# Optimization experiments

Hardware: AMD Instinct MI355X
Metric: run time of the kernel (lower is better)

The kernel has to match this reference:

```python
import jax, jax.numpy as jnp
import numpy as np

D_MODEL = 256
D_STATE = 32
D_CONV = 16
EXPAND = 4
N_LAYERS = 4
D_INNER = EXPAND * D_MODEL  # 1024
DT_RANK = 16  # ceil(d_model / 16)
INPUT_DIM = 78
BATCH = 4096
EPS = 1e-5


def setup_inputs() -> dict:
    key = jax.random.key(0)
    ks = jax.random.split(key, 10)
    f = lambda k, shape, s: jax.random.normal(k, shape, jnp.float32) * s
    return {
        "x": f(ks[0], (BATCH, INPUT_DIM), 1.0),
        "W_proj_in": f(ks[1], (INPUT_DIM, D_MODEL), 0.1),
        "b_proj_in": jnp.zeros((D_MODEL,), jnp.float32),
        "norm_w": jnp.ones((N_LAYERS, D_MODEL), jnp.float32),
        "W_in": f(ks[2], (N_LAYERS, D_MODEL, 2 * D_INNER), 0.05),
        "conv_w": f(ks[3], (N_LAYERS, D_INNER, D_CONV), 0.2),
        "conv_b": jnp.zeros((N_LAYERS, D_INNER), jnp.float32),
        "W_x": f(ks[4], (N_LAYERS, D_INNER, DT_RANK + 2 * D_STATE), 0.03),
        "W_dt": f(ks[5], (N_LAYERS, DT_RANK, D_INNER), 0.1),
        "b_dt": f(ks[6], (N_LAYERS, D_INNER), 0.1),
        "A_log": jnp.log(jnp.broadcast_to(jnp.arange(1, D_STATE + 1, dtype=jnp.float32), (N_LAYERS, D_INNER, D_STATE))),
        "D": jnp.ones((N_LAYERS, D_INNER), jnp.float32),
        "W_out": f(ks[7], (N_LAYERS, D_INNER, D_MODEL), 0.03),
        "W_final": f(ks[8], (D_MODEL, 1), 0.06),
        "b_final": jnp.zeros((1,), jnp.float32),
    }


def _rmsnorm(x, w):
    return x * jax.lax.rsqrt(jnp.mean(x * x, axis=-1, keepdims=True) + EPS) * w


def _causal_dwconv(x, w, b):
    # x: [B, L, ED], w: [ED, K] depthwise causal conv (left pad K-1)
    lhs = jnp.transpose(x, (0, 2, 1))                 # [B, ED, L]
    rhs = w[:, None, :]                               # [ED, 1, K]
    out = jax.lax.conv_general_dilated(lhs, rhs, (1,), [(D_CONV - 1, 0)], feature_group_count=D_INNER)
    return jnp.transpose(out, (0, 2, 1)) + b


def _ssm(x, Wx, Wdt, bdt, A_log, Dp):
    # x: [B, L, ED]
    A = -jnp.exp(A_log)                               # [ED, N]
    dbc = x @ Wx                                      # [B, L, dt_rank + 2N]
    delta = jax.nn.softplus(dbc[..., :DT_RANK] @ Wdt + bdt)   # [B, L, ED]
    Bm = dbc[..., DT_RANK:DT_RANK + D_STATE]          # [B, L, N]
    Cm = dbc[..., DT_RANK + D_STATE:]                 # [B, L, N]
    dA = jnp.exp(delta[..., None] * A)                # [B, L, ED, N]
    dBx = (delta * x)[..., None] * Bm[:, :, None, :]  # [B, L, ED, N]

    def step(h, inp):
        a, bx = inp
        h = a * h + bx
        return h, h

    h0 = jnp.zeros((x.shape[0], D_INNER, D_STATE), x.dtype)
    _, hs = jax.lax.scan(step, h0, (jnp.moveaxis(dA, 1, 0), jnp.moveaxis(dBx, 1, 0)))  # hs: [L, B, ED, N]
    y = jnp.einsum('lben,bln->ble', hs, Cm)           # [B, L, ED]
    return y + Dp * x


def _mamba_block(x, W_in, cw, cb, Wx, Wdt, bdt, A_log, Dp, W_out):
    xz = x @ W_in                                     # [B, L, 2*ED]
    xi, z = jnp.split(xz, 2, axis=-1)
    xi = jax.nn.silu(_causal_dwconv(xi, cw, cb))
    y = _ssm(xi, Wx, Wdt, bdt, A_log, Dp)
    y = y * jax.nn.silu(z)
    return y @ W_out


def reference(x, W_proj_in, b_proj_in, norm_w, W_in, conv_w, conv_b, W_x, W_dt, b_dt, A_log, D, W_out, W_final, b_final):
    h = (x @ W_proj_in + b_proj_in)[:, None, :]       # [B, 1, d_model]
    for l in range(N_LAYERS):
        h = h + _mamba_block(_rmsnorm(h, norm_w[l]), W_in[l], conv_w[l], conv_b[l],
                             W_x[l], W_dt[l], b_dt[l], A_log[l], D[l], W_out[l])
    h = h[:, 0, :]
    return jax.nn.sigmoid(h @ W_final + b_final)      # [B, 1]
```

## Files before the change

### kernel.cpp

```cpp
#include <hip/hip_runtime.h>
#include <hip/hip_bf16.h>
#include <math.h>

#define BATCH 4096
#define IDIM 78
#define DM 256
#define DI 1024
#define NL 4

typedef __attribute__((ext_vector_type(8))) short bf16x8;
typedef __attribute__((ext_vector_type(4))) float f32x4;

__device__ __forceinline__ float siluf(float v){ return v / (1.0f + __expf(-v)); }
__device__ __forceinline__ float softplusf(float v){
  return fmaxf(v, 0.f) + __logf(1.f + __expf(-fabsf(v)));
}
__device__ __forceinline__ ushort f2bf(float f){
  union { float f; unsigned u; } c; c.f = f;
  unsigned r = c.u + 0x7fff + ((c.u >> 16) & 1);
  return (ushort)(r >> 16);
}
__device__ __forceinline__ float bf2f(ushort b){
  union { unsigned u; float f; } c; c.u = ((unsigned)b) << 16; return c.f;
}
__device__ __forceinline__ unsigned pack2(float lo, float hi){
  return (unsigned)f2bf(lo) | ((unsigned)f2bf(hi) << 16);
}
__device__ __forceinline__ void async_copy16(void* lds, const void* g){
  __builtin_amdgcn_global_load_lds(
      (const __attribute__((address_space(1))) unsigned int*)g,
      (__attribute__((address_space(3))) unsigned int*)lds, 16, 0, 0);
}

__global__ __launch_bounds__(256) void k_pre(const float* __restrict__ Win,
    const float* __restrict__ Wout, const float* __restrict__ Wx,
    ushort* __restrict__ WinT, ushort* __restrict__ WoutT, ushort* __restrict__ WxT,
    const float* __restrict__ x, const float* __restrict__ Wp,
    const float* __restrict__ bp, const float* __restrict__ nw,
    float* __restrict__ h, ushort* __restrict__ xn){
  __shared__ __align__(16) char smem[17408];
  int bid = blockIdx.x, t = threadIdx.x;
  if (bid < 768){
    float (*tl)[65] = (float(*)[65])smem;
    const float* src; ushort* dst; int R, C, r0, c0;
    if (bid < 512){
      int l = bid>>7, b = bid&127;
      src = Win + (size_t)l*DM*2*DI;  dst = WinT + (size_t)l*2*DI*DM;
      R = DM; C = 2*DI; r0 = (b>>5)*64; c0 = (b&31)*64;
    } else {
      int b2 = bid-512; int l = b2>>6, b = b2&63;
      src = Wout + (size_t)l*DI*DM;   dst = WoutT + (size_t)l*DM*DI;
      R = DI; C = DM; r0 = (b>>2)*64; c0 = (b&3)*64;
    }
    int ci4 = (t&15)*4, rq = t>>4;
    #pragma unroll
    for (int p=0;p<4;p++){
      int ri = p*16+rq;
      float4 v = *(const float4*)(src + (size_t)(r0+ri)*C + c0+ci4);
      tl[ri][ci4]=v.x; tl[ri][ci4+1]=v.y; tl[ri][ci4+2]=v.z; tl[ri][ci4+3]=v.w;
    }
    __syncthreads();
    int ci2 = (t&31)*2, rq2 = t>>5;
    #pragma unroll
    for (int p=0;p<8;p++){
      int ri = p*8+rq2;
      *(unsigned*)(dst + (size_t)(c0+ri)*R + r0+ci2) = pack2(tl[ci2][ri], tl[ci2+1][ri]);
    }
  } else if (bid < 848){
    float* lw = (float*)smem;
    int b = bid-768; int l = b/20, y0 = (b%20)*4;
    const float* src = Wx + (size_t)l*DI*80 + y0;
    #pragma unroll
    for (int p=0;p<4;p++){
      int k = p*256+t;
      float4 v = *(const float4*)(src + (size_t)k*80);
      lw[k] = v.x; lw[1040+k] = v.y; lw[2080+k] = v.z; lw[3120+k] = v.w;
    }
    __syncthreads();
    int yi = t>>6, kk = (t&63)*16;
    const float* s = lw + yi*1040 + kk;
    ushort* dr = WxT + (size_t)l*80*DI + (size_t)(y0+yi)*DI + kk;
    uint4 o0, o1;
    o0.x = pack2(s[ 0],s[ 1]); o0.y = pack2(s[ 2],s[ 3]);
    o0.z = pack2(s[ 4],s[ 5]); o0.w = pack2(s[ 6],s[ 7]);
    o1.x = pack2(s[ 8],s[ 9]); o1.y = pack2(s[10],s[11]);
    o1.z = pack2(s[12],s[13]); o1.w = pack2(s[14],s[15]);
    *(uint4*)dr = o0; *(uint4*)(dr+8) = o1;
  } else {
    float (*xs)[80] = (float(*)[80])smem;
    float (*sred)[4] = (float(*)[4])(smem + 5120);
    float* ssc = (float*)(smem + 5376);
    int row0 = (bid - 848)*16;
    int wid = t>>6;
    if (t < IDIM){
      #pragma unroll
      for (int r=0;r<16;r++) xs[r][t] = x[(size_t)(row0+r)*IDIM + t];
    }
    __syncthreads();
    int col = t;
    float acc[16];
    float b0 = bp[col];
    #pragma unroll
    for (int r=0;r<16;r++) acc[r] = b0;
    for (int k=0;k<IDIM;k++){
      float wv = Wp[k*DM + col];
      #pragma unroll
      for (int r=0;r<16;r++) acc[r] = fmaf(xs[r][k], wv, acc[r]);
    }
    #pragma unroll
    for (int r=0;r<16;r++){
      float sq = acc[r]*acc[r];
      #pragma unroll
      for (int o=32;o>0;o>>=1) sq += __shfl_xor(sq, o);
      if ((t&63)==0) sred[r][wid] = sq;
    }
    __syncthreads();
    if (t < 16){
      float tot = sred[t][0]+sred[t][1]+sred[t][2]+sred[t][3];
      ssc[t] = rsqrtf(tot*(1.0f/DM) + 1e-5f);
    }
    __syncthreads();
    float nwv = nw[col];
    #pragma unroll
    for (int r=0;r<16;r++){
      size_t o = (size_t)(row0+r)*DM + col;
      h[o] = acc[r];
      xn[o] = f2bf(acc[r]*ssc[r]*nwv);
    }
  }
}

__global__ __launch_bounds__(128, 4) void k_blk0(
    const ushort* __restrict__ A,
    const ushort* __restrict__ Bt,
    const float* __restrict__ cwl, const float* __restrict__ cbl,
    ushort* __restrict__ xi, ushort* __restrict__ sz)
{
  __shared__ __align__(16) ushort lds[12288];
  int t = threadIdx.x, w = t>>6, lane = t&63;
  int lr = lane&15, lk = lane>>4;
  int row0 = blockIdx.x*64, col0 = blockIdx.y*128;
  int srow = lane>>2;
  int ssw = (lane&3) ^ ((lane>>3)&3);
  const ushort* Ag = A  + (size_t)(row0 + srow)*DM + ssw*8;
  const ushort* Bg = Bt + (size_t)(col0 + srow)*DM + ssw*8;
  int rsw = (lk ^ ((lr>>1)&3))*8;

  #define AS(buf) (lds + (buf)*2048)
  #define BS(buf) (lds + 4096 + (buf)*4096)
  #define STAGE(buf, tt) { \
    int ko = (tt)*32; \
    if (w == 0){ \
      _Pragma("unroll") \
      for (int q=0;q<4;q++) async_copy16(AS(buf) + q*512, Ag + (size_t)q*16*DM + ko); \
      _Pragma("unroll") \
      for (int c=0;c<2;c++) async_copy16(BS(buf) + c*512, Bg + (size_t)c*16*DM + ko); \
    } else { \
      _Pragma("unroll") \
      for (int c=2;c<8;c++) async_copy16(BS(buf) + c*512, Bg + (size_t)c*16*DM + ko); \
    } }

  f32x4 acc[4][4] = {};
  STAGE(0, 0);
  __syncthreads();
  int cur = 0;
  #pragma unroll
  for (int tt=0; tt<8; ++tt){
    if (tt < 7) STAGE(cur^1, tt+1);
    bf16x8 av[4], bv[4];
    #pragma unroll
    for (int i=0;i<4;i++) av[i] = *(const bf16x8*)(AS(cur) + (i*16+lr)*32 + rsw);
    #pragma unroll
    for (int j=0;j<4;j++) bv[j] = *(const bf16x8*)(BS(cur) + (w*64 + j*16+lr)*32 + rsw);
    #pragma unroll
    for (int i=0;i<4;i++)
      #pragma unroll
      for (int j=0;j<4;j++)
        acc[i][j] = __builtin_amdgcn_mfma_f32_16x16x32_bf16(av[i], bv[j], acc[i][j], 0,0,0);
    __syncthreads();
    cur ^= 1;
  }

  const bool is_xi = (col0 < DI);
  float scw[4], scb[4];
  if (is_xi){
    #pragma unroll
    for (int j=0;j<4;j++){
      int colb = col0 + w*64 + j*16 + lr;
      scw[j] = cwl[colb*16+15];
      scb[j] = cbl[colb];
    }
  }
  ushort* cs = lds;
  #pragma unroll
  for (int i=0;i<4;i++)
    #pragma unroll
    for (int j=0;j<4;j++){
      int cl = w*64 + j*16 + lr;
      #pragma unroll
      for (int r=0;r<4;r++){
        int rl = i*16 + lk*4 + r;
        float v = acc[i][j][r];
        cs[rl*136 + cl] = f2bf(is_xi ? siluf(fmaf(scw[j], v, scb[j])) : siluf(v));
      }
    }
  __syncthreads();
  int rl = t>>1, half = t&1;
  ushort* drow = (is_xi ? (xi + col0) : (sz + col0 - DI)) + (size_t)(row0+rl)*DI + half*64;
  const ushort* srcr = cs + rl*136 + half*64;
  #pragma unroll
  for (int u=0;u<8;u++)
    *(uint4*)&drow[u*8] = *(const uint4*)&srcr[u*8];
  #undef AS
  #undef BS
  #undef STAGE
}

__global__ __launch_bounds__(512) void k_ssm(const ushort* __restrict__ xi, const ushort* __restrict__ sz,
    const ushort* __restrict__ WxT, const float* __restrict__ Wdt, const float* __restrict__ bdt,
    const float* __restrict__ Dd, ushort* __restrict__ y){
  __shared__ float dsum[8][16][81];
  __shared__ __align__(16) float dbcc[16][16];
  __shared__ float sS[16];
  int r0 = blockIdx.x*16;
  int t = threadIdx.x, w = t>>6, lane = t&63, lr = lane&15, lk = lane>>4;
  f32x4 acc[5] = {};
  const ushort* Ab = xi  + (size_t)(r0+lr)*DI + w*128 + lk*8;
  const ushort* Bb = WxT + (size_t)lr*DI      + w*128 + lk*8;
  #pragma unroll
  for (int s=0;s<4;s++){
    bf16x8 a = *(const bf16x8*)(Ab + s*32);
    #pragma unroll
    for (int j=0;j<5;j++){
      bf16x8 b = *(const bf16x8*)(Bb + (size_t)j*16*DI + s*32);
      acc[j] = __builtin_amdgcn_mfma_f32_16x16x32_bf16(a, b, acc[j], 0,0,0);
    }
  }
  #pragma unroll
  for (int j=0;j<5;j++)
    #pragma unroll
    for (int r=0;r<4;r++)
      dsum[w][lk*4+r][j*16+lr] = acc[j][r];
  __syncthreads();
  for (int idx=t; idx<16*80; idx+=512){
    int rr = idx/80, n = idx%80;
    float s = dsum[0][rr][n];
    #pragma unroll
    for (int q=1;q<8;q++) s += dsum[q][rr][n];
    dsum[0][rr][n] = s;
    if (n < 16) dbcc[rr][n] = s;
  }
  __syncthreads();
  if (t < 256){
    int row = t>>4, ln = t&15;
    float p = dsum[0][row][16+ln]*dsum[0][row][48+ln]
            + dsum[0][row][32+ln]*dsum[0][row][64+ln];
    p += __shfl_xor(p, 8); p += __shfl_xor(p, 4); p += __shfl_xor(p, 2); p += __shfl_xor(p, 1);
    if (ln==0) sS[row] = p;
  }
  __syncthreads();
  int e = 2*t;
  float2 wdtr[16];
  #pragma unroll
  for (int r=0;r<16;r++) wdtr[r] = *(const float2*)(Wdt + (size_t)r*DI + e);
  float2 bd = *(const float2*)(bdt + e);
  float2 dd = *(const float2*)(Dd + e);
  for (int row=0; row<16; ++row){
    float4 d0 = *(const float4*)&dbcc[row][0];
    float4 d1 = *(const float4*)&dbcc[row][4];
    float4 d2 = *(const float4*)&dbcc[row][8];
    float4 d3 = *(const float4*)&dbcc[row][12];
    float u0 = bd.x, u1 = bd.y;
    u0 = fmaf(wdtr[ 0].x, d0.x, u0); u1 = fmaf(wdtr[ 0].y, d0.x, u1);
    u0 = fmaf(wdtr[ 1].x, d0.y, u0); u1 = fmaf(wdtr[ 1].y, d0.y, u1);
    u0 = fmaf(wdtr[ 2].x, d0.z, u0); u1 = fmaf(wdtr[ 2].y, d0.z, u1);
    u0 = fmaf(wdtr[ 3].x, d0.w, u0); u1 = fmaf(wdtr[ 3].y, d0.w, u1);
    u0 = fmaf(wdtr[ 4].x, d1.x, u0); u1 = fmaf(wdtr[ 4].y, d1.x, u1);
    u0 = fmaf(wdtr[ 5].x, d1.y, u0); u1 = fmaf(wdtr[ 5].y, d1.y, u1);
    u0 = fmaf(wdtr[ 6].x, d1.z, u0); u1 = fmaf(wdtr[ 6].y, d1.z, u1);
    u0 = fmaf(wdtr[ 7].x, d1.w, u0); u1 = fmaf(wdtr[ 7].y, d1.w, u1);
    u0 = fmaf(wdtr[ 8].x, d2.x, u0); u1 = fmaf(wdtr[ 8].y, d2.x, u1);
    u0 = fmaf(wdtr[ 9].x, d2.y, u0); u1 = fmaf(wdtr[ 9].y, d2.y, u1);
    u0 = fmaf(wdtr[10].x, d2.z, u0); u1 = fmaf(wdtr[10].y, d2.z, u1);
    u0 = fmaf(wdtr[11].x, d2.w, u0); u1 = fmaf(wdtr[11].y, d2.w, u1);
    u0 = fmaf(wdtr[12].x, d3.x, u0); u1 = fmaf(wdtr[12].y, d3.x, u1);
    u0 = fmaf(wdtr[13].x, d3.y, u0); u1 = fmaf(wdtr[13].y, d3.y, u1);
    u0 = fmaf(wdtr[14].x, d3.z, u0); u1 = fmaf(wdtr[14].y, d3.z, u1);
    u0 = fmaf(wdtr[15].x, d3.w, u0); u1 = fmaf(wdtr[15].y, d3.w, u1);
    float srow = sS[row];
    float dl0 = softplusf(u0), dl1 = softplusf(u1);
    size_t o = (size_t)(r0+row)*DI + e;
    ushort2 xv = *(const ushort2*)(xi + o);
    ushort2 zv = *(const ushort2*)(sz + o);
    ushort2 ov;
    ov.x = f2bf(bf2f(xv.x) * fmaf(dl0, srow, dd.x) * bf2f(zv.x));
    ov.y = f2bf(bf2f(xv.y) * fmaf(dl1, srow, dd.y) * bf2f(zv.y));
    *(ushort2*)(y + o) = ov;
  }
}

__global__ __launch_bounds__(256) void k_blk1(
    const ushort* __restrict__ A,
    const ushort* __restrict__ Bt,
    float* __restrict__ h)
{
  __shared__ __align__(16) ushort As[32][256];
  __shared__ __align__(16) ushort Bs[64][256];
  int t = threadIdx.x, wid = t>>6, lane = t&63;
  int wr = wid>>1, wc = wid&1, lr = lane&15, lk = lane>>4;
  int row0 = blockIdx.x*32, col0 = blockIdx.y*64;
  int lrow = lane>>5, lch = lane&31;
  f32x4 acc[2] = {};

  for (int kc=0; kc<4; ++kc){
    int ko = kc*256;
    #pragma unroll
    for (int q=0;q<4;q++){
      int rr = wid*8 + q*2 + lrow;
      async_copy16(&As[wid*8 + q*2][0], A  + (size_t)(row0+rr)*DI + ko + ((lch ^ (rr&7))<<3));
    }
    #pragma unroll
    for (int q=0;q<8;q++){
      int rr = wid*16 + q*2 + lrow;
      async_copy16(&Bs[wid*16 + q*2][0], Bt + (size_t)(col0+rr)*DI + ko + ((lch ^ (rr&7))<<3));
    }
    __syncthreads();
    #pragma unroll
    for (int kk=0;kk<8;kk++){
      int rr = wr*16 + lr;
      bf16x8 a = *(const bf16x8*)&As[rr][(((kk<<2)|lk) ^ (rr&7))<<3];
      #pragma unroll
      for (int j=0;j<2;j++){
        int cc = wc*32 + j*16 + lr;
        bf16x8 b = *(const bf16x8*)&Bs[cc][(((kk<<2)|lk) ^ (cc&7))<<3];
        acc[j] = __builtin_amdgcn_mfma_f32_16x16x32_bf16(a, b, acc[j], 0,0,0);
      }
    }
    __syncthreads();
  }

  float* ls = (float*)&As[0][0];
  #pragma unroll
  for (int j=0;j<2;j++){
    int cl = wc*32 + j*16 + lr;
    #pragma unroll
    for (int r=0;r<4;r++)
      ls[(wr*16 + lk*4 + r)*68 + cl] = acc[j][r];
  }
  __syncthreads();
  int rl = t>>3, c8 = (t&7)*8;
  size_t o = (size_t)(row0+rl)*DM + col0 + c8;
  #pragma unroll
  for (int p=0;p<2;p++){
    float4 add = *(float4*)&ls[rl*68 + c8 + p*4];
    float4 hv = *(float4*)&h[o + p*4];
    hv.x += add.x; hv.y += add.y; hv.z += add.z; hv.w += add.w;
    *(float4*)&h[o + p*4] = hv;
  }
}

template<int LAST>
__global__ __launch_bounds__(256) void k_norm(const float* __restrict__ h,
    const float* __restrict__ nw, const float* __restrict__ Wf,
    const float* __restrict__ bf, ushort* __restrict__ xn, float* __restrict__ out){
  __shared__ float sred[16][4];
  __shared__ float sfin[16][4];
  __shared__ float ssc[16];
  int row0 = blockIdx.x*16;
  int t = threadIdx.x, wid = t>>6;
  float v[16];
  #pragma unroll
  for (int r=0;r<16;r++) v[r] = h[(size_t)(row0+r)*DM + t];
  float wf = 0.f;
  if constexpr (LAST) wf = Wf[t];
  #pragma unroll
  for (int r=0;r<16;r++){
    float sq = v[r]*v[r];
    float pf = LAST ? v[r]*wf : 0.f;
    #pragma unroll
    for (int o=32;o>0;o>>=1){
      sq += __shfl_xor(sq, o);
      if constexpr (LAST) pf += __shfl_xor(pf, o);
    }
    if ((t&63)==0){ sred[r][wid] = sq; if constexpr (LAST) sfin[r][wid] = pf; }
  }
  __syncthreads();
  if (t < 16){
    float tot = sred[t][0]+sred[t][1]+sred[t][2]+sred[t][3];
    ssc[t] = rsqrtf(tot*(1.0f/DM) + 1e-5f);
    if constexpr (LAST){
      float ft = sfin[t][0]+sfin[t][1]+sfin[t][2]+sfin[t][3];
      out[row0 + t] = 1.0f/(1.0f + __expf(-(ft + bf[0])));
    }
  }
  __syncthreads();
  if constexpr (!LAST){
    float nwv = nw[t];
    #pragma unroll
    for (int r=0;r<16;r++)
      xn[(size_t)(row0+r)*DM + t] = f2bf(v[r]*ssc[r]*nwv);
  }
}

extern "C" void kernel_launch(void* const* d_in, const int* in_sizes, int n_in,
                              void* d_out, int out_size, void* d_ws, size_t ws_size,
                              hipStream_t stream){
  const float* x   = (const float*)d_in[0];
  const float* Wp  = (const float*)d_in[1];
  const float* bp  = (const float*)d_in[2];
  const float* nw  = (const float*)d_in[3];
  const float* Win = (const float*)d_in[4];
  const float* cw  = (const float*)d_in[5];
  const float* cb  = (const float*)d_in[6];
  const float* Wx  = (const float*)d_in[7];
  const float* Wdt = (const float*)d_in[8];
  const float* bdt = (const float*)d_in[9];
  const float* Dd  = (const float*)d_in[11];
  const float* Wout= (const float*)d_in[12];
  const float* Wf  = (const float*)d_in[13];
  const float* bf  = (const float*)d_in[14];
  float* out = (float*)d_out;

  char* wsb = (char*)d_ws;
  float*  h    = (float*)wsb;  wsb += (size_t)BATCH*DM*4;
  ushort* xn   = (ushort*)wsb; wsb += (size_t)BATCH*DM*2;
  ushort* xi   = (ushort*)wsb; wsb += (size_t)BATCH*DI*2;
  ushort* sz   = (ushort*)wsb; wsb += (size_t)BATCH*DI*2;
  ushort* WinT = (ushort*)wsb; wsb += (size_t)NL*2*DI*DM*2;
  ushort* WoutT= (ushort*)wsb; wsb += (size_t)NL*DM*DI*2;
  ushort* WxT  = (ushort*)wsb; wsb += (size_t)NL*80*DI*2;

  k_pre<<<1104, 256, 0, stream>>>(Win, Wout, Wx, WinT, WoutT, WxT,
                                  x, Wp, bp, nw, h, xn);
  for (int l=0;l<NL;l++){
    k_blk0<<<dim3(BATCH/64, (2*DI)/128), 128, 0, stream>>>(
        xn, WinT + (size_t)l*2*DI*DM,
        cw + (size_t)l*DI*16, cb + (size_t)l*DI, xi, sz);
    k_ssm<<<BATCH/16, 512, 0, stream>>>(xi, sz, WxT + (size_t)l*80*DI,
        Wdt + (size_t)l*16*DI, bdt + (size_t)l*DI, Dd + (size_t)l*DI, xi);
    k_blk1<<<dim3(BATCH/32, DM/64), 256, 0, stream>>>(
        xi, WoutT + (size_t)l*DM*DI, h);
    if (l < NL-1)
      k_norm<0><<<BATCH/16, 256, 0, stream>>>(h, nw + (l+1)*DM, nullptr, nullptr, xn, nullptr);
    else
      k_norm<1><<<BATCH/16, 256, 0, stream>>>(h, nullptr, Wf, bf, nullptr, out);
  }
}
```

Measured before the change: 209.7 us.

## Double-buffer out-projection GEMM with smaller K tiles to overlap loads

```diff
diff --git a/kernel.cpp b/kernel.cpp
--- a/kernel.cpp
+++ b/kernel.cpp
@@ -304,42 +304,47 @@
     const ushort* __restrict__ Bt,
     float* __restrict__ h)
 {
-  __shared__ __align__(16) ushort As[32][256];
-  __shared__ __align__(16) ushort Bs[64][256];
+  __shared__ __align__(16) ushort lds[12288];
   int t = threadIdx.x, wid = t>>6, lane = t&63;
   int wr = wid>>1, wc = wid&1, lr = lane&15, lk = lane>>4;
   int row0 = blockIdx.x*32, col0 = blockIdx.y*64;
-  int lrow = lane>>5, lch = lane&31;
+  int srow8 = lane>>3;
+  int ssw = (lane&7) ^ srow8;
+  const ushort* Agw = A  + (size_t)(row0 + wid*8 + srow8)*DI + ssw*8;
+  const ushort* Bg0 = Bt + (size_t)(col0 + wid*16 + srow8)*DI + ssw*8;
+
+  #define AS1(buf) (lds + (buf)*6144)
+  #define BS1(buf) (lds + (buf)*6144 + 2048)
+  #define STAGE1(buf, tt) { \
+    int ko = (tt)*64; \
+    async_copy16(AS1(buf) + wid*8*64, Agw + ko); \
+    _Pragma("unroll") \
+    for (int q=0;q<2;q++) async_copy16(BS1(buf) + (wid*16 + q*8)*64, Bg0 + (size_t)q*8*DI + ko); }
+
   f32x4 acc[2] = {};
-
-  for (int kc=0; kc<4; ++kc){
-    int ko = kc*256;
-    #pragma unroll
-    for (int q=0;q<4;q++){
-      int rr = wid*8 + q*2 + lrow;
-      async_copy16(&As[wid*8 + q*2][0], A  + (size_t)(row0+rr)*DI + ko + ((lch ^ (rr&7))<<3));
-    }
-    #pragma unroll
-    for (int q=0;q<8;q++){
-      int rr = wid*16 + q*2 + lrow;
-      async_copy16(&Bs[wid*16 + q*2][0], Bt + (size_t)(col0+rr)*DI + ko + ((lch ^ (rr&7))<<3));
-    }
-    __syncthreads();
-    #pragma unroll
-    for (int kk=0;kk<8;kk++){
-      int rr = wr*16 + lr;
-      bf16x8 a = *(const bf16x8*)&As[rr][(((kk<<2)|lk) ^ (rr&7))<<3];
+  STAGE1(0, 0);
+  __syncthreads();
+  int cur = 0;
+  #pragma unroll
+  for (int tt=0; tt<16; ++tt){
+    if (tt < 15) STAGE1(cur^1, tt+1);
+    #pragma unroll
+    for (int s=0;s<2;s++){
+      int arow = wr*16 + lr;
+      int slotA = ((s*4+lk) ^ (lr&7))*8;
+      bf16x8 a = *(const bf16x8*)(AS1(cur) + arow*64 + slotA);
       #pragma unroll
       for (int j=0;j<2;j++){
-        int cc = wc*32 + j*16 + lr;
-        bf16x8 b = *(const bf16x8*)&Bs[cc][(((kk<<2)|lk) ^ (cc&7))<<3];
+        int brow = wc*32 + j*16 + lr;
+        bf16x8 b = *(const bf16x8*)(BS1(cur) + brow*64 + slotA);
         acc[j] = __builtin_amdgcn_mfma_f32_16x16x32_bf16(a, b, acc[j], 0,0,0);
       }
     }
     __syncthreads();
-  }
-
-  float* ls = (float*)&As[0][0];
+    cur ^= 1;
+  }
+
+  float* ls = (float*)lds;
   #pragma unroll
   for (int j=0;j<2;j++){
     int cl = wc*32 + j*16 + lr;
@@ -357,6 +362,9 @@
     hv.x += add.x; hv.y += add.y; hv.z += add.z; hv.w += add.w;
     *(float4*)&h[o + p*4] = hv;
   }
+  #undef AS1
+  #undef BS1
+  #undef STAGE1
 }
 
 template<int LAST>
```

Result: slower. 215.5 us (+2.8%).

## Fold RMSNorm into in-projection GEMM epilogue and drop per-layer norm kernel

Applied to the files above, without the earlier changes.

```diff
diff --git a/kernel.cpp b/kernel.cpp
--- a/kernel.cpp
+++ b/kernel.cpp
@@ -34,19 +34,22 @@
 
 __global__ __launch_bounds__(256) void k_pre(const float* __restrict__ Win,
     const float* __restrict__ Wout, const float* __restrict__ Wx,
+    const float* __restrict__ nw,
     ushort* __restrict__ WinT, ushort* __restrict__ WoutT, ushort* __restrict__ WxT,
     const float* __restrict__ x, const float* __restrict__ Wp,
-    const float* __restrict__ bp, const float* __restrict__ nw,
-    float* __restrict__ h, ushort* __restrict__ xn){
+    const float* __restrict__ bp,
+    float* __restrict__ h, ushort* __restrict__ hb, float* __restrict__ pssq){
   __shared__ __align__(16) char smem[17408];
   int bid = blockIdx.x, t = threadIdx.x;
   if (bid < 768){
     float (*tl)[65] = (float(*)[65])smem;
     const float* src; ushort* dst; int R, C, r0, c0;
+    const float* nwl = nullptr;
     if (bid < 512){
       int l = bid>>7, b = bid&127;
       src = Win + (size_t)l*DM*2*DI;  dst = WinT + (size_t)l*2*DI*DM;
       R = DM; C = 2*DI; r0 = (b>>5)*64; c0 = (b&31)*64;
+      nwl = nw + l*DM;
     } else {
       int b2 = bid-512; int l = b2>>6, b = b2&63;
       src = Wout + (size_t)l*DI*DM;   dst = WoutT + (size_t)l*DM*DI;
@@ -57,7 +60,8 @@
     for (int p=0;p<4;p++){
       int ri = p*16+rq;
       float4 v = *(const float4*)(src + (size_t)(r0+ri)*C + c0+ci4);
-      tl[ri][ci4]=v.x; tl[ri][ci4+1]=v.y; tl[ri][ci4+2]=v.z; tl[ri][ci4+3]=v.w;
+      float s = nwl ? nwl[r0+ri] : 1.0f;
+      tl[ri][ci4]=v.x*s; tl[ri][ci4+1]=v.y*s; tl[ri][ci4+2]=v.z*s; tl[ri][ci4+3]=v.w*s;
     }
     __syncthreads();
     int ci2 = (t&31)*2, rq2 = t>>5;
@@ -89,7 +93,6 @@
   } else {
     float (*xs)[80] = (float(*)[80])smem;
     float (*sred)[4] = (float(*)[4])(smem + 5120);
-    float* ssc = (float*)(smem + 5376);
     int row0 = (bid - 848)*16;
     int wid = t>>6;
     if (t < IDIM){
@@ -114,29 +117,30 @@
       for (int o=32;o>0;o>>=1) sq += __shfl_xor(sq, o);
       if ((t&63)==0) sred[r][wid] = sq;
     }
-    __syncthreads();
-    if (t < 16){
-      float tot = sred[t][0]+sred[t][1]+sred[t][2]+sred[t][3];
-      ssc[t] = rsqrtf(tot*(1.0f/DM) + 1e-5f);
-    }
-    __syncthreads();
-    float nwv = nw[col];
     #pragma unroll
     for (int r=0;r<16;r++){
       size_t o = (size_t)(row0+r)*DM + col;
       h[o] = acc[r];
-      xn[o] = f2bf(acc[r]*ssc[r]*nwv);
+      hb[o] = f2bf(acc[r]);
+    }
+    __syncthreads();
+    if (t < 16){
+      int row = row0 + t;
+      pssq[row] = sred[t][0]+sred[t][1]+sred[t][2]+sred[t][3];
+      pssq[BATCH+row] = 0.f; pssq[2*BATCH+row] = 0.f; pssq[3*BATCH+row] = 0.f;
     }
   }
 }
 
 __global__ __launch_bounds__(128, 4) void k_blk0(
     const ushort* __restrict__ A,
+    const float* __restrict__ pq,
     const ushort* __restrict__ Bt,
     const float* __restrict__ cwl, const float* __restrict__ cbl,
     ushort* __restrict__ xi, ushort* __restrict__ sz)
 {
   __shared__ __align__(16) ushort lds[12288];
+  __shared__ float ssc_l[64];
   int t = threadIdx.x, w = t>>6, lane = t&63;
   int lr = lane&15, lk = lane>>4;
   int row0 = blockIdx.x*64, col0 = blockIdx.y*128;
@@ -145,6 +149,12 @@
   const ushort* Ag = A  + (size_t)(row0 + srow)*DM + ssw*8;
   const ushort* Bg = Bt + (size_t)(col0 + srow)*DM + ssw*8;
   int rsw = (lk ^ ((lr>>1)&3))*8;
+
+  if (t < 64){
+    int row = row0 + t;
+    float s = pq[row] + pq[BATCH+row] + pq[2*BATCH+row] + pq[3*BATCH+row];
+    ssc_l[t] = rsqrtf(s*(1.0f/DM) + 1e-5f);
+  }
 
   #define AS(buf) (lds + (buf)*2048)
   #define BS(buf) (lds + 4096 + (buf)*4096)
@@ -200,7 +210,7 @@
       #pragma unroll
       for (int r=0;r<4;r++){
         int rl = i*16 + lk*4 + r;
-        float v = acc[i][j][r];
+        float v = acc[i][j][r] * ssc_l[rl];
         cs[rl*136 + cl] = f2bf(is_xi ? siluf(fmaf(scw[j], v, scb[j])) : siluf(v));
       }
     }
@@ -302,7 +312,7 @@
 __global__ __launch_bounds__(256) void k_blk1(
     const ushort* __restrict__ A,
     const ushort* __restrict__ Bt,
-    float* __restrict__ h)
+    float* __restrict__ h, ushort* __restrict__ hb, float* __restrict__ pssq)
 {
   __shared__ __align__(16) ushort As[32][256];
   __shared__ __align__(16) ushort Bs[64][256];
@@ -350,55 +360,46 @@
   __syncthreads();
   int rl = t>>3, c8 = (t&7)*8;
   size_t o = (size_t)(row0+rl)*DM + col0 + c8;
-  #pragma unroll
-  for (int p=0;p<2;p++){
-    float4 add = *(float4*)&ls[rl*68 + c8 + p*4];
-    float4 hv = *(float4*)&h[o + p*4];
-    hv.x += add.x; hv.y += add.y; hv.z += add.z; hv.w += add.w;
-    *(float4*)&h[o + p*4] = hv;
-  }
-}
-
-template<int LAST>
-__global__ __launch_bounds__(256) void k_norm(const float* __restrict__ h,
-    const float* __restrict__ nw, const float* __restrict__ Wf,
-    const float* __restrict__ bf, ushort* __restrict__ xn, float* __restrict__ out){
-  __shared__ float sred[16][4];
+  float4 hv0, hv1;
+  {
+    float4 add = *(float4*)&ls[rl*68 + c8];
+    hv0 = *(float4*)&h[o];
+    hv0.x += add.x; hv0.y += add.y; hv0.z += add.z; hv0.w += add.w;
+    *(float4*)&h[o] = hv0;
+  }
+  {
+    float4 add = *(float4*)&ls[rl*68 + c8 + 4];
+    hv1 = *(float4*)&h[o + 4];
+    hv1.x += add.x; hv1.y += add.y; hv1.z += add.z; hv1.w += add.w;
+    *(float4*)&h[o + 4] = hv1;
+  }
+  uint4 hw;
+  hw.x = pack2(hv0.x, hv0.y); hw.y = pack2(hv0.z, hv0.w);
+  hw.z = pack2(hv1.x, hv1.y); hw.w = pack2(hv1.z, hv1.w);
+  *(uint4*)(hb + o) = hw;
+  float sq = hv0.x*hv0.x + hv0.y*hv0.y + hv0.z*hv0.z + hv0.w*hv0.w
+           + hv1.x*hv1.x + hv1.y*hv1.y + hv1.z*hv1.z + hv1.w*hv1.w;
+  sq += __shfl_xor(sq, 1); sq += __shfl_xor(sq, 2); sq += __shfl_xor(sq, 4);
+  if ((t&7)==0) pssq[(size_t)blockIdx.y*BATCH + row0 + rl] = sq;
+}
+
+__global__ __launch_bounds__(256) void k_final(const float* __restrict__ h,
+    const float* __restrict__ Wf, const float* __restrict__ bf, float* __restrict__ out){
   __shared__ float sfin[16][4];
-  __shared__ float ssc[16];
   int row0 = blockIdx.x*16;
   int t = threadIdx.x, wid = t>>6;
-  float v[16];
-  #pragma unroll
-  for (int r=0;r<16;r++) v[r] = h[(size_t)(row0+r)*DM + t];
-  float wf = 0.f;
-  if constexpr (LAST) wf = Wf[t];
+  float wf = Wf[t];
   #pragma unroll
   for (int r=0;r<16;r++){
-    float sq = v[r]*v[r];
-    float pf = LAST ? v[r]*wf : 0.f;
-    #pragma unroll
-    for (int o=32;o>0;o>>=1){
-      sq += __shfl_xor(sq, o);
-      if constexpr (LAST) pf += __shfl_xor(pf, o);
-    }
-    if ((t&63)==0){ sred[r][wid] = sq; if constexpr (LAST) sfin[r][wid] = pf; }
+    float pf = h[(size_t)(row0+r)*DM + t] * wf;
+    #pragma unroll
+    for (int o=32;o>0;o>>=1) pf += __shfl_xor(pf, o);
+    if ((t&63)==0) sfin[r][wid] = pf;
   }
   __syncthreads();
   if (t < 16){
-    float tot = sred[t][0]+sred[t][1]+sred[t][2]+sred[t][3];
-    ssc[t] = rsqrtf(tot*(1.0f/DM) + 1e-5f);
-    if constexpr (LAST){
-      float ft = sfin[t][0]+sfin[t][1]+sfin[t][2]+sfin[t][3];
-      out[row0 + t] = 1.0f/(1.0f + __expf(-(ft + bf[0])));
-    }
-  }
-  __syncthreads();
-  if constexpr (!LAST){
-    float nwv = nw[t];
-    #pragma unroll
-    for (int r=0;r<16;r++)
-      xn[(size_t)(row0+r)*DM + t] = f2bf(v[r]*ssc[r]*nwv);
+    float ft = sfin[t][0]+sfin[t][1]+sfin[t][2]+sfin[t][3];
+    out[row0 + t] = 1.0f/(1.0f + __expf(-(ft + bf[0])));
   }
 }
 
@@ -423,26 +424,24 @@
 
   char* wsb = (char*)d_ws;
   float*  h    = (float*)wsb;  wsb += (size_t)BATCH*DM*4;
-  ushort* xn   = (ushort*)wsb; wsb += (size_t)BATCH*DM*2;
+  ushort* hb   = (ushort*)wsb; wsb += (size_t)BATCH*DM*2;
   ushort* xi   = (ushort*)wsb; wsb += (size_t)BATCH*DI*2;
   ushort* sz   = (ushort*)wsb; wsb += (size_t)BATCH*DI*2;
   ushort* WinT = (ushort*)wsb; wsb += (size_t)NL*2*DI*DM*2;
   ushort* WoutT= (ushort*)wsb; wsb += (size_t)NL*DM*DI*2;
   ushort* WxT  = (ushort*)wsb; wsb += (size_t)NL*80*DI*2;
-
-  k_pre<<<1104, 256, 0, stream>>>(Win, Wout, Wx, WinT, WoutT, WxT,
-                                  x, Wp, bp, nw, h, xn);
+  float*  pssq = (float*)wsb;  wsb += (size_t)4*BATCH*4;
+
+  k_pre<<<1104, 256, 0, stream>>>(Win, Wout, Wx, nw, WinT, WoutT, WxT,
+                                  x, Wp, bp, h, hb, pssq);
   for (int l=0;l<NL;l++){
     k_blk0<<<dim3(BATCH/64, (2*DI)/128), 128, 0, stream>>>(
-        xn, WinT + (size_t)l*2*DI*DM,
+        hb, pssq, WinT + (size_t)l*2*DI*DM,
         cw + (size_t)l*DI*16, cb + (size_t)l*DI, xi, sz);
     k_ssm<<<BATCH/16, 512, 0, stream>>>(xi, sz, WxT + (size_t)l*80*DI,
         Wdt + (size_t)l*16*DI, bdt + (size_t)l*DI, Dd + (size_t)l*DI, xi);
     k_blk1<<<dim3(BATCH/32, DM/64), 256, 0, stream>>>(
-        xi, WoutT + (size_t)l*DM*DI, h);
-    if (l < NL-1)
-      k_norm<0><<<BATCH/16, 256, 0, stream>>>(h, nw + (l+1)*DM, nullptr, nullptr, xn, nullptr);
-    else
-      k_norm<1><<<BATCH/16, 256, 0, stream>>>(h, nullptr, Wf, bf, nullptr, out);
-  }
-}
+        xi, WoutT + (size_t)l*DM*DI, h, hb, pssq);
+  }
+  k_final<<<BATCH/16, 256, 0, stream>>>(h, Wf, bf, out);
+}
```

Result: faster. 201.8 us (-3.8%).
